# Kernel tuning notes

Hardware: AMD Instinct MI355X
Metric: run time of the kernel (lower is better)

The kernel has to match this reference:

```python
import jax, jax.numpy as jnp
import numpy as np

B, S, D, H, E, K = 2, 2048, 512, 2048, 16, 2
LN_EPS = 1e-5


def setup_inputs() -> dict:
    key = jax.random.key(0)
    ks = jax.random.split(key, 9)
    s_in = 1.0 / np.sqrt(D)
    s_hid = 1.0 / np.sqrt(H)
    return {
        "x": jax.random.normal(ks[0], (B, S, D), dtype=jnp.float32),
        "Wg": jax.random.normal(ks[1], (D, E), dtype=jnp.float32) * s_in,
        "bg": jax.random.normal(ks[2], (E,), dtype=jnp.float32) * 0.01,
        "W1": jax.random.normal(ks[3], (E, D, H), dtype=jnp.float32) * s_in,
        "b1": jax.random.normal(ks[4], (E, H), dtype=jnp.float32) * 0.01,
        "W2": jax.random.normal(ks[5], (E, H, D), dtype=jnp.float32) * s_hid,
        "b2": jax.random.normal(ks[6], (E, D), dtype=jnp.float32) * 0.01,
        "gamma": jnp.ones((D,), dtype=jnp.float32),
        "beta": jnp.zeros((D,), dtype=jnp.float32),
    }


def reference(x, Wg, bg, W1, b1, W2, b2, gamma, beta):
    # --- top-k gating (GatingFuncTopK) ---
    logits = jnp.einsum("bsd,de->bse", x, Wg) + bg            # [B,S,E]
    probs = jax.nn.softmax(logits, axis=-1)
    topk_vals, topk_idx = jax.lax.top_k(probs, K)             # [B,S,K]
    # scatter top-k probs back into a sparse [B,S,E] routing matrix
    sparse = (jax.nn.one_hot(topk_idx, E, dtype=probs.dtype)
              * topk_vals[..., None]).sum(axis=-2)            # [B,S,E]

    # --- dense all-expert FFN (stack over experts, as in the torch code) ---
    h = jax.nn.relu(jnp.einsum("bsd,edh->ebsh", x, W1)
                    + b1[:, None, None, :])                   # [E,B,S,H]
    ex = jnp.einsum("ebsh,ehd->ebsd", h, W2) + b2[:, None, None, :]  # [E,B,S,D]

    # --- weighted combine + residual + layernorm ---
    out = jnp.einsum("bse,ebsd->bsd", sparse, ex) + x
    mu = out.mean(axis=-1, keepdims=True)
    var = ((out - mu) ** 2).mean(axis=-1, keepdims=True)
    out = (out - mu) * jax.lax.rsqrt(var + LN_EPS) * gamma + beta
    return out
```

## Files before the change

### kernel.cpp

```cpp
#include <hip/hip_runtime.h>
#include <math.h>

#define NTOK 4096
#define DDIM 512
#define HDIM 2048
#define NEXP 16


#define WS_COUNTS    0u
#define WS_OFFSETS   1024u
#define WS_NTILES    1280u
#define WS_TM        1536u
#define WS_EPOS      4096u
#define WS_TOK       36864u
#define WS_WL        299008u
#define WS_XA        1048576u
#define WS_W1T       11534336u
#define WS_W2T       45088768u
#define WS_HB        78643200u
#define WS_YB        WS_W1T

typedef __attribute__((ext_vector_type(8))) short short8;
typedef __attribute__((ext_vector_type(4))) float floatx4;
typedef unsigned short ushort_t;

__device__ __forceinline__ ushort_t f2bf(float f) {
    unsigned u = __float_as_uint(f);
    u += 0x7fffu + ((u >> 16) & 1u);
    return (ushort_t)(u >> 16);
}
__device__ __forceinline__ float bf2f(ushort_t u) {
    return __uint_as_float((unsigned)u << 16);
}

__device__ __forceinline__ void gld16(const void* g, void* l) {
    __builtin_amdgcn_global_load_lds(
        (const __attribute__((address_space(1))) unsigned*)g,
        (__attribute__((address_space(3))) unsigned*)l, 16, 0, 0);
}

__device__ __forceinline__ void wtrans_tile(
    const float* __restrict__ src, ushort_t* __restrict__ dst,
    int C, int NT, int CK, int e, int ks, int nw, unsigned* lb, int tid)
{
    const int q = tid >> 4;
    const int c0 = (tid & 15) << 2;
    const float* sp = src + (size_t)e * (DDIM * HDIM)
                    + (size_t)(ks * 32 + 2 * q) * C + nw * 256;
    float4 va[4], vb[4];
    #pragma unroll
    for (int p = 0; p < 4; ++p) {
        va[p] = *(const float4*)(sp + c0 + p * 64);
        vb[p] = *(const float4*)(sp + C + c0 + p * 64);
    }
    #pragma unroll
    for (int p = 0; p < 4; ++p) {
        const int n = c0 + p * 64;
        lb[(n + 0) * 17 + q] = (unsigned)f2bf(va[p].x) | ((unsigned)f2bf(vb[p].x) << 16);
        lb[(n + 1) * 17 + q] = (unsigned)f2bf(va[p].y) | ((unsigned)f2bf(vb[p].y) << 16);
        lb[(n + 2) * 17 + q] = (unsigned)f2bf(va[p].z) | ((unsigned)f2bf(vb[p].z) << 16);
        lb[(n + 3) * 17 + q] = (unsigned)f2bf(va[p].w) | ((unsigned)f2bf(vb[p].w) << 16);
    }
    __syncthreads();
    const int nt = tid >> 4, nl = tid & 15;
    const int ntg = nw * 16 + nt;
    ushort_t* rbase = dst + ((size_t)e * NT + ntg) * ((size_t)CK * 128) + nl * 8;
    const unsigned* rp = lb + (nt * 16 + nl) * 17;
    #pragma unroll
    for (int kc = 0; kc < 4; ++kc) {
        const unsigned o0 = rp[kc * 4 + 0], o1 = rp[kc * 4 + 1];
        const unsigned o2 = rp[kc * 4 + 2], o3 = rp[kc * 4 + 3];
        *(uint4*)(rbase + (size_t)(ks * 4 + kc) * 128) = make_uint4(o0, o1, o2, o3);
    }
}

__global__ __launch_bounds__(256) void fusedA_kernel(
    const float* __restrict__ x, const float* __restrict__ Wg,
    const float* __restrict__ bg, int* __restrict__ counts,
    int* __restrict__ tok_list, float* __restrict__ w_list,
    int* __restrict__ epos, const float* __restrict__ W1,
    ushort_t* __restrict__ W1t)
{
    __shared__ __align__(16) float smem[4416];
    __shared__ int lcnt[16], lbase[16];
    const int tid = threadIdx.x;
    int bid = blockIdx.x;

    if (bid >= 512) {
        bid -= 512;
        const int e = bid >> 7, r = bid & 127;
        const int nw = r & 7, ks = r >> 3;
        wtrans_tile(W1, W1t, HDIM, 128, 64, e, ks, nw, (unsigned*)smem, tid);
        return;
    }

    float (*xs)[520] = (float(*)[520])smem;
    float (*lsm)[16][2] = (float(*)[16][2])(smem + 4160);
    const int t0 = bid * 8;
    const float* xg = x + (size_t)t0 * DDIM;
    #pragma unroll
    for (int p = 0; p < 4; ++p) {
        const int idx = p * 1024 + tid * 4;
        *(float4*)&xs[idx >> 9][idx & 511] = *(const float4*)(xg + idx);
    }
    if (tid < 16) lcnt[tid] = 0;
    __syncthreads();
    const int tl = tid >> 5, e = (tid >> 1) & 15, h = tid & 1;
    float a0 = 0.f, a1 = 0.f, a2 = 0.f, a3 = 0.f;
    #pragma unroll 8
    for (int it = 0; it < 64; ++it) {
        const int d = h * 256 + it * 4;
        const float4 xv = *(const float4*)&xs[tl][d];
        a0 = fmaf(xv.x, Wg[(d + 0) * 16 + e], a0);
        a1 = fmaf(xv.y, Wg[(d + 1) * 16 + e], a1);
        a2 = fmaf(xv.z, Wg[(d + 2) * 16 + e], a2);
        a3 = fmaf(xv.w, Wg[(d + 3) * 16 + e], a3);
    }
    lsm[tl][e][h] = (a0 + a1) + (a2 + a3);
    __syncthreads();

    int i0 = 0, i1 = -1, r0 = 0, r1 = 0;
    float w0 = 0.f, w1 = 0.f;
    const bool tokth = ((tid & 31) == 0);
    if (tokth) {
        float l[16];
        #pragma unroll
        for (int j = 0; j < NEXP; ++j) l[j] = lsm[tl][j][0] + lsm[tl][j][1] + bg[j];
        float m = -1e30f;
        #pragma unroll
        for (int j = 0; j < NEXP; ++j) m = fmaxf(m, l[j]);
        float s = 0.f;
        #pragma unroll
        for (int j = 0; j < NEXP; ++j) s += __expf(l[j] - m);
        float v0 = -1e30f;
        #pragma unroll
        for (int j = 0; j < NEXP; ++j)
            if (l[j] > v0) { v0 = l[j]; i0 = j; }
        float v1 = -1e30f;
        #pragma unroll
        for (int j = 0; j < NEXP; ++j)
            if (j != i0 && l[j] > v1) { v1 = l[j]; i1 = j; }
        w0 = __expf(v0 - m) / s;
        w1 = __expf(v1 - m) / s;
        r0 = atomicAdd(&lcnt[i0], 1);
        r1 = atomicAdd(&lcnt[i1], 1);
    }
    __syncthreads();
    if (tid < 16 && lcnt[tid] > 0)
        lbase[tid] = atomicAdd(&counts[tid * 16], lcnt[tid]);
    __syncthreads();
    if (tokth) {
        const int t = t0 + tl;
        const int p0 = lbase[i0] + r0;
        tok_list[i0 * NTOK + p0] = t;
        w_list[i0 * NTOK + p0] = w0;
        epos[t * 2 + 0] = (i0 << 16) | p0;
        const int p1 = lbase[i1] + r1;
        tok_list[i1 * NTOK + p1] = t;
        w_list[i1 * NTOK + p1] = w1;
        epos[t * 2 + 1] = (i1 << 16) | p1;
    }
}

__global__ void scan_kernel(const int* __restrict__ counts, int* __restrict__ offsets,
                            int* __restrict__ tm, int* __restrict__ ntiles)
{
    const int lane = threadIdx.x;
    int c = (lane < NEXP) ? counts[lane * 16] : 0;
    int t = (c + 127) >> 7;
    int ic = c, it = t;
    #pragma unroll
    for (int off = 1; off < 16; off <<= 1) {
        const int pc = __shfl_up(ic, off, 64);
        const int pt = __shfl_up(it, off, 64);
        if (lane >= off) { ic += pc; it += pt; }
    }
    if (lane < NEXP) {
        offsets[lane] = ic - c;
        if (lane == NEXP - 1) { offsets[NEXP] = ic; ntiles[0] = it; }
        const int tb = it - t;
        for (int i = 0; i < t; ++i) tm[tb + i] = (lane << 16) | i;
    }
}

__global__ __launch_bounds__(256) void gather_xa(
    const float* __restrict__ x, const int* __restrict__ tok_list,
    const int* __restrict__ counts, const int* __restrict__ tm,
    const int* __restrict__ ntiles, ushort_t* __restrict__ xa)
{
    const int b = blockIdx.x;
    if (b >= ntiles[0]) return;
    const int info = tm[b];
    const int e = info >> 16, m0 = (info & 0xffff) << 7;
    const int Me = counts[e * 16];
    const int row = threadIdx.x >> 1;
    const int half = threadIdx.x & 1;
    const int kbase = blockIdx.y * 128 + half * 64;
    const int tok = tok_list[e * NTOK + min(m0 + row, Me - 1)];
    const float* src = x + (size_t)tok * DDIM + kbase;
    ushort_t* dstb = xa + (size_t)b * 65536 + (size_t)(row >> 4) * 8192 + (row & 15) * 8;
    #pragma unroll
    for (int q = 0; q < 16; ++q) {
        const int k = kbase + q * 4;
        const float4 v = *(const float4*)(src + q * 4);
        ushort4 o = make_ushort4(f2bf(v.x), f2bf(v.y), f2bf(v.z), f2bf(v.w));
        *(ushort4*)(dstb + (size_t)(k >> 3) * 128 + (k & 7)) = o;
    }
}

__global__ __launch_bounds__(256) void fusedC_kernel(
    const ushort_t* __restrict__ xa, const ushort_t* __restrict__ W1t,
    const float* __restrict__ b1, const int* __restrict__ tm,
    const int* __restrict__ ntiles, ushort_t* __restrict__ hb,
    const float* __restrict__ W2, ushort_t* __restrict__ W2t)
{
    __shared__ __align__(16) ushort_t lds[16384];
    const int tid = threadIdx.x;
    const int bid = blockIdx.x;

    if (bid >= 1280) {
        const int wb = bid - 1280;
        const int e = wb >> 7, r = wb & 127;
        const int nw = r & 1, ks = r >> 1;
        wtrans_tile(W2, W2t, DDIM, 32, 256, e, ks, nw, (unsigned*)lds, tid);
        return;
    }

    const int t = bid >> 4;
    if (t >= ntiles[0]) return;
    const int e = tm[t] >> 16;
    const int n0 = (bid & 15) << 7;
    const int lane = tid & 63, w = tid >> 6;
    const int fm = lane & 15, fq = lane >> 4;
    const int wr = (w >> 1) << 6, wc = (w & 1) << 6;

    const ushort_t* gA = xa + (size_t)t * 65536 + lane * 8;
    const ushort_t* gB = W1t + ((size_t)e * 128 + (n0 >> 4)) * 8192 + lane * 8;
    const int s0 = w, s1 = w + 4;

    #define G1_STAGE(d, kc) do {                                            \
        ushort_t* lb_ = &lds[(d) * 8192];                                   \
        gld16(gA + (size_t)s0 * 8192 + (kc) * 512, lb_ + s0 * 512);         \
        gld16(gA + (size_t)s1 * 8192 + (kc) * 512, lb_ + s1 * 512);         \
        gld16(gB + (size_t)s0 * 8192 + (kc) * 512, lb_ + 4096 + s0 * 512);  \
        gld16(gB + (size_t)s1 * 8192 + (kc) * 512, lb_ + 4096 + s1 * 512);  \
    } while (0)

    G1_STAGE(0, 0);
    __syncthreads();

    floatx4 acc[4][4] = {};
    for (int kc = 0; kc < 16; ++kc) {
        const int d = kc & 1;
        if (kc < 15) G1_STAGE(d ^ 1, kc + 1);
        const ushort_t* la = &lds[d * 8192 + (wr >> 4) * 512 + lane * 8];
        const ushort_t* lbB = &lds[d * 8192 + 4096 + (wc >> 4) * 512 + lane * 8];
        short8 af[4], bf[4];
        #pragma unroll
        for (int i = 0; i < 4; ++i) af[i] = *(const short8*)(la + i * 512);
        #pragma unroll
        for (int j = 0; j < 4; ++j) bf[j] = *(const short8*)(lbB + j * 512);
        #pragma unroll
        for (int i = 0; i < 4; ++i)
            #pragma unroll
            for (int j = 0; j < 4; ++j)
                acc[i][j] = __builtin_amdgcn_mfma_f32_16x16x32_bf16(
                    af[i], bf[j], acc[i][j], 0, 0, 0);
        __syncthreads();
    }
    #undef G1_STAGE

    ushort_t* ls = lds;
    #pragma unroll
    for (int j = 0; j < 4; ++j) {
        const float bias = b1[(size_t)e * HDIM + n0 + wc + j * 16 + fm];
        #pragma unroll
        for (int i = 0; i < 4; ++i)
            #pragma unroll
            for (int r = 0; r < 4; ++r) {
                const int row = wr + i * 16 + fq * 4 + r;
                ls[row * 128 + wc + j * 16 + fm] =
                    f2bf(fmaxf(acc[i][j][r] + bias, 0.f));
            }
    }
    __syncthreads();
    ushort_t* hbase = hb + (size_t)t * 262144 + (size_t)(n0 >> 3) * 128;
    #pragma unroll
    for (int p = 0; p < 8; ++p) {
        const int unit = tid + p * 256;
        const int row = unit >> 4, c16 = unit & 15;
        *(short8*)(hbase + (size_t)(row >> 4) * 32768 + (size_t)c16 * 128
                   + (row & 15) * 8) = *(const short8*)&ls[row * 128 + c16 * 8];
    }
}

__global__ __launch_bounds__(256) void gemm2_mfma(
    const ushort_t* __restrict__ hb, const ushort_t* __restrict__ W2t,
    const float* __restrict__ b2, const float* __restrict__ w_list,
    const int* __restrict__ counts, const int* __restrict__ offsets,
    const int* __restrict__ tm, const int* __restrict__ ntiles,
    ushort_t* __restrict__ yb)
{
    const int t = blockIdx.y;
    if (t >= ntiles[0]) return;
    const int info = tm[t];
    const int e = info >> 16, m0 = (info & 0xffff) << 7;
    const int Me = counts[e * 16], aoff = offsets[e];
    const int n0 = blockIdx.x << 7;
    const int kz = blockIdx.z;
    const int tid = threadIdx.x, lane = tid & 63, w = tid >> 6;
    const int fm = lane & 15, fq = lane >> 4;
    const int wr = (w >> 1) << 6, wc = (w & 1) << 6;

    __shared__ __align__(16) ushort_t lds[16384];

    const ushort_t* gA = hb + (size_t)t * 262144 + (size_t)kz * 8192 + lane * 8;
    const ushort_t* gB = W2t + ((size_t)e * 32 + (n0 >> 4)) * 32768
                       + (size_t)kz * 8192 + lane * 8;
    const int s0 = w, s1 = w + 4;

    #define G2_STAGE(d, kc) do {                                            \
        ushort_t* lb_ = &lds[(d) * 8192];                                   \
        gld16(gA + (size_t)s0 * 32768 + (kc) * 512, lb_ + s0 * 512);        \
        gld16(gA + (size_t)s1 * 32768 + (kc) * 512, lb_ + s1 * 512);        \
        gld16(gB + (size_t)s0 * 32768 + (kc) * 512, lb_ + 4096 + s0 * 512); \
        gld16(gB + (size_t)s1 * 32768 + (kc) * 512, lb_ + 4096 + s1 * 512); \
    } while (0)

    G2_STAGE(0, 0);
    __syncthreads();

    floatx4 acc[4][4] = {};
    for (int kc = 0; kc < 16; ++kc) {
        const int d = kc & 1;
        if (kc < 15) G2_STAGE(d ^ 1, kc + 1);
        const ushort_t* la = &lds[d * 8192 + (wr >> 4) * 512 + lane * 8];
        const ushort_t* lbB = &lds[d * 8192 + 4096 + (wc >> 4) * 512 + lane * 8];
        short8 af[4], bf[4];
        #pragma unroll
        for (int i = 0; i < 4; ++i) af[i] = *(const short8*)(la + i * 512);
        #pragma unroll
        for (int j = 0; j < 4; ++j) bf[j] = *(const short8*)(lbB + j * 512);
        #pragma unroll
        for (int i = 0; i < 4; ++i)
            #pragma unroll
            for (int j = 0; j < 4; ++j)
                acc[i][j] = __builtin_amdgcn_mfma_f32_16x16x32_bf16(
                    af[i], bf[j], acc[i][j], 0, 0, 0);
        __syncthreads();
    }
    #undef G2_STAGE

    ushort_t* ls = lds;
    #pragma unroll
    for (int j = 0; j < 4; ++j) {
        const float bias = (kz == 0) ? b2[(size_t)e * DDIM + n0 + wc + j * 16 + fm] : 0.f;
        #pragma unroll
        for (int i = 0; i < 4; ++i)
            #pragma unroll
            for (int r = 0; r < 4; ++r) {
                const int row = wr + i * 16 + fq * 4 + r;
                const float gw = w_list[e * NTOK + min(m0 + row, Me - 1)];
                ls[row * 128 + wc + j * 16 + fm] = f2bf(gw * (acc[i][j][r] + bias));
            }
    }
    __syncthreads();
    ushort_t* ybase = yb + (size_t)kz * (8192 * 512) + n0;
    #pragma unroll
    for (int p = 0; p < 8; ++p) {
        const int unit = tid + p * 256;
        const int row = unit >> 4, c16 = unit & 15;
        if (m0 + row < Me)
            *(short8*)(ybase + (size_t)(aoff + m0 + row) * 512 + c16 * 8)
                = *(const short8*)&ls[row * 128 + c16 * 8];
    }
}

__global__ __launch_bounds__(256) void ln_kernel(
    const float* __restrict__ x, const ushort_t* __restrict__ yb,
    const int* __restrict__ epos, const int* __restrict__ offsets,
    const float* __restrict__ gamma, const float* __restrict__ beta,
    float* __restrict__ out)
{
    const int t = blockIdx.x * 4 + (threadIdx.x >> 6);
    const int lane = threadIdx.x & 63;
    const int d0 = lane * 8;

    const int p0 = epos[2 * t + 0];
    const int p1 = epos[2 * t + 1];
    const size_t r0 = (size_t)(offsets[p0 >> 16] + (p0 & 0xFFFF));
    const size_t r1 = (size_t)(offsets[p1 >> 16] + (p1 & 0xFFFF));

    short8 ys[8];
    #pragma unroll
    for (int kz = 0; kz < 4; ++kz) {
        ys[kz * 2 + 0] = *(const short8*)(yb + (size_t)kz * (8192 * 512) + r0 * 512 + d0);
        ys[kz * 2 + 1] = *(const short8*)(yb + (size_t)kz * (8192 * 512) + r1 * 512 + d0);
    }
    float xv[8];
    *(float4*)&xv[0] = *(const float4*)(x + (size_t)t * DDIM + d0);
    *(float4*)&xv[4] = *(const float4*)(x + (size_t)t * DDIM + d0 + 4);

    float v[8];
    float s = 0.f;
    #pragma unroll
    for (int i = 0; i < 8; ++i) {
        float a = xv[i];
        #pragma unroll
        for (int q = 0; q < 8; ++q) a += bf2f((ushort_t)ys[q][i]);
        v[i] = a;
        s += a;
    }
    #pragma unroll
    for (int o = 32; o > 0; o >>= 1) s += __shfl_xor(s, o, 64);
    const float mu = s * (1.f / DDIM);
    float q = 0.f;
    #pragma unroll
    for (int i = 0; i < 8; ++i) { const float d_ = v[i] - mu; q = fmaf(d_, d_, q); }
    #pragma unroll
    for (int o = 32; o > 0; o >>= 1) q += __shfl_xor(q, o, 64);
    const float rstd = rsqrtf(q * (1.f / DDIM) + 1e-5f);

    float g[8], bt[8], o8[8];
    *(float4*)&g[0] = *(const float4*)(gamma + d0);
    *(float4*)&g[4] = *(const float4*)(gamma + d0 + 4);
    *(float4*)&bt[0] = *(const float4*)(beta + d0);
    *(float4*)&bt[4] = *(const float4*)(beta + d0 + 4);
    #pragma unroll
    for (int i = 0; i < 8; ++i) o8[i] = (v[i] - mu) * rstd * g[i] + bt[i];
    *(float4*)(out + (size_t)t * DDIM + d0) = *(float4*)&o8[0];
    *(float4*)(out + (size_t)t * DDIM + d0 + 4) = *(float4*)&o8[4];
}

extern "C" void kernel_launch(void* const* d_in, const int* in_sizes, int n_in,
                              void* d_out, int out_size, void* d_ws, size_t ws_size,
                              hipStream_t stream) {
    const float* x     = (const float*)d_in[0];
    const float* Wg    = (const float*)d_in[1];
    const float* bg    = (const float*)d_in[2];
    const float* W1    = (const float*)d_in[3];
    const float* b1    = (const float*)d_in[4];
    const float* W2    = (const float*)d_in[5];
    const float* b2    = (const float*)d_in[6];
    const float* gamma = (const float*)d_in[7];
    const float* beta  = (const float*)d_in[8];
    float* out = (float*)d_out;

    char* ws = (char*)d_ws;
    int*      counts   = (int*)(ws + WS_COUNTS);
    int*      offsets  = (int*)(ws + WS_OFFSETS);
    int*      ntiles   = (int*)(ws + WS_NTILES);
    int*      tm       = (int*)(ws + WS_TM);
    int*      epos     = (int*)(ws + WS_EPOS);
    int*      tok_list = (int*)(ws + WS_TOK);
    float*    w_list   = (float*)(ws + WS_WL);
    ushort_t* xa       = (ushort_t*)(ws + WS_XA);
    ushort_t* W1t      = (ushort_t*)(ws + WS_W1T);
    ushort_t* W2t      = (ushort_t*)(ws + WS_W2T);
    ushort_t* hb       = (ushort_t*)(ws + WS_HB);
    ushort_t* yb       = (ushort_t*)(ws + WS_YB);

    hipMemsetAsync(counts, 0, 1024, stream);
    fusedA_kernel<<<2560, 256, 0, stream>>>(x, Wg, bg, counts, tok_list, w_list,
                                            epos, W1, W1t);
    scan_kernel<<<1, 64, 0, stream>>>(counts, offsets, tm, ntiles);
    gather_xa<<<dim3(80, 4), 256, 0, stream>>>(x, tok_list, counts, tm, ntiles, xa);
    fusedC_kernel<<<3328, 256, 0, stream>>>(xa, W1t, b1, tm, ntiles, hb, W2, W2t);
    gemm2_mfma<<<dim3(DDIM / 128, 80, 4), 256, 0, stream>>>(
        hb, W2t, b2, w_list, counts, offsets, tm, ntiles, yb);
    ln_kernel<<<NTOK / 4, 256, 0, stream>>>(x, yb, epos, offsets, gamma, beta, out);
}
```

Baseline: 276.5 us.

## Triple-buffer GEMM K-loop with vmcnt waits and swizzle block indices

Both expert GEMM kernels move from a double-buffered LDS pipeline with full syncthreads to a three-stage ring buffer. Each stage waits with an explicit s_waitcnt vmcnt(4) plus barrier, so two async global-to-LDS loads stay in flight while MFMA work runs. Block IDs are remapped with an 8-way XCD-style swizzle, and gemm2 now uses a flat 1D grid, to improve cache locality across chiplets. This raises LDS use per block to 48KB, which may lower occupancy, and relies on hand-counted vmcnt values being correct.

Result: faster. 263.2 us (-4.8%).

```diff
diff --git a/kernel.cpp b/kernel.cpp
--- a/kernel.cpp
+++ b/kernel.cpp
@@ -39,6 +39,9 @@
         (__attribute__((address_space(3))) unsigned*)l, 16, 0, 0);
 }
 
+#define WAIT4_BAR() asm volatile("s_waitcnt vmcnt(4)\n\ts_barrier" ::: "memory")
+#define WAIT0_BAR() asm volatile("s_waitcnt vmcnt(0)\n\ts_barrier" ::: "memory")
+
 __device__ __forceinline__ void wtrans_tile(
     const float* __restrict__ src, ushort_t* __restrict__ dst,
     int C, int NT, int CK, int e, int ks, int nw, unsigned* lb, int tid)
@@ -214,7 +217,7 @@
     const int* __restrict__ ntiles, ushort_t* __restrict__ hb,
     const float* __restrict__ W2, ushort_t* __restrict__ W2t)
 {
-    __shared__ __align__(16) ushort_t lds[16384];
+    __shared__ __align__(16) ushort_t lds[24576];
     const int tid = threadIdx.x;
     const int bid = blockIdx.x;
 
@@ -226,10 +229,11 @@
         return;
     }
 
-    const int t = bid >> 4;
+    const int swz = (bid & 7) * 160 + (bid >> 3);
+    const int t = swz >> 4;
     if (t >= ntiles[0]) return;
     const int e = tm[t] >> 16;
-    const int n0 = (bid & 15) << 7;
+    const int n0 = (swz & 15) << 7;
     const int lane = tid & 63, w = tid >> 6;
     const int fm = lane & 15, fq = lane >> 4;
     const int wr = (w >> 1) << 6, wc = (w & 1) << 6;
@@ -246,29 +250,42 @@
         gld16(gB + (size_t)s1 * 8192 + (kc) * 512, lb_ + 4096 + s1 * 512);  \
     } while (0)
 
+    #define G1_COMPUTE(cur) do {                                            \
+        const ushort_t* la = &lds[(cur) * 8192 + ((w >> 1) * 4) * 512 + lane * 8]; \
+        const ushort_t* lbB = &lds[(cur) * 8192 + 4096 + ((w & 1) * 4) * 512 + lane * 8]; \
+        short8 af[4], bf[4];                                                \
+        _Pragma("unroll")                                                   \
+        for (int i = 0; i < 4; ++i) af[i] = *(const short8*)(la + i * 512); \
+        _Pragma("unroll")                                                   \
+        for (int j = 0; j < 4; ++j) bf[j] = *(const short8*)(lbB + j * 512);\
+        _Pragma("unroll")                                                   \
+        for (int i = 0; i < 4; ++i)                                         \
+            _Pragma("unroll")                                               \
+            for (int j = 0; j < 4; ++j)                                     \
+                acc[i][j] = __builtin_amdgcn_mfma_f32_16x16x32_bf16(        \
+                    af[i], bf[j], acc[i][j], 0, 0, 0);                      \
+    } while (0)
+
     G1_STAGE(0, 0);
-    __syncthreads();
-
+    G1_STAGE(1, 1);
     floatx4 acc[4][4] = {};
-    for (int kc = 0; kc < 16; ++kc) {
-        const int d = kc & 1;
-        if (kc < 15) G1_STAGE(d ^ 1, kc + 1);
-        const ushort_t* la = &lds[d * 8192 + (wr >> 4) * 512 + lane * 8];
-        const ushort_t* lbB = &lds[d * 8192 + 4096 + (wc >> 4) * 512 + lane * 8];
-        short8 af[4], bf[4];
-        #pragma unroll
-        for (int i = 0; i < 4; ++i) af[i] = *(const short8*)(la + i * 512);
-        #pragma unroll
-        for (int j = 0; j < 4; ++j) bf[j] = *(const short8*)(lbB + j * 512);
-        #pragma unroll
-        for (int i = 0; i < 4; ++i)
-            #pragma unroll
-            for (int j = 0; j < 4; ++j)
-                acc[i][j] = __builtin_amdgcn_mfma_f32_16x16x32_bf16(
-                    af[i], bf[j], acc[i][j], 0, 0, 0);
-        __syncthreads();
-    }
+    int cur = 0;
+    #pragma unroll 1
+    for (int kc = 0; kc < 14; ++kc) {
+        WAIT4_BAR();
+        const int nb = (kc + 2) % 3;
+        G1_STAGE(nb, kc + 2);
+        G1_COMPUTE(cur);
+        cur = (cur == 2) ? 0 : cur + 1;
+    }
+    WAIT4_BAR();
+    G1_COMPUTE(cur);
+    cur = (cur == 2) ? 0 : cur + 1;
+    WAIT0_BAR();
+    G1_COMPUTE(cur);
+    __syncthreads();
     #undef G1_STAGE
+    #undef G1_COMPUTE
 
     ushort_t* ls = lds;
     #pragma unroll
@@ -301,18 +318,22 @@
     const int* __restrict__ tm, const int* __restrict__ ntiles,
     ushort_t* __restrict__ yb)
 {
-    const int t = blockIdx.y;
+    const int bid = blockIdx.x;
+    const int swz = (bid & 7) * 160 + (bid >> 3);
+    const int n0i = swz & 3;
+    const int q = swz >> 2;
+    const int kz = q / 80;
+    const int t = q - kz * 80;
     if (t >= ntiles[0]) return;
     const int info = tm[t];
     const int e = info >> 16, m0 = (info & 0xffff) << 7;
     const int Me = counts[e * 16], aoff = offsets[e];
-    const int n0 = blockIdx.x << 7;
-    const int kz = blockIdx.z;
+    const int n0 = n0i << 7;
     const int tid = threadIdx.x, lane = tid & 63, w = tid >> 6;
     const int fm = lane & 15, fq = lane >> 4;
     const int wr = (w >> 1) << 6, wc = (w & 1) << 6;
 
-    __shared__ __align__(16) ushort_t lds[16384];
+    __shared__ __align__(16) ushort_t lds[24576];
 
     const ushort_t* gA = hb + (size_t)t * 262144 + (size_t)kz * 8192 + lane * 8;
     const ushort_t* gB = W2t + ((size_t)e * 32 + (n0 >> 4)) * 32768
@@ -327,29 +348,42 @@
         gld16(gB + (size_t)s1 * 32768 + (kc) * 512, lb_ + 4096 + s1 * 512); \
     } while (0)
 
+    #define G2_COMPUTE(cur) do {                                            \
+        const ushort_t* la = &lds[(cur) * 8192 + ((w >> 1) * 4) * 512 + lane * 8]; \
+        const ushort_t* lbB = &lds[(cur) * 8192 + 4096 + ((w & 1) * 4) * 512 + lane * 8]; \
+        short8 af[4], bf[4];                                                \
+        _Pragma("unroll")                                                   \
+        for (int i = 0; i < 4; ++i) af[i] = *(const short8*)(la + i * 512); \
+        _Pragma("unroll")                                                   \
+        for (int j = 0; j < 4; ++j) bf[j] = *(const short8*)(lbB + j * 512);\
+        _Pragma("unroll")                                                   \
+        for (int i = 0; i < 4; ++i)                                         \
+            _Pragma("unroll")                                               \
+            for (int j = 0; j < 4; ++j)                                     \
+                acc[i][j] = __builtin_amdgcn_mfma_f32_16x16x32_bf16(        \
+                    af[i], bf[j], acc[i][j], 0, 0, 0);                      \
+    } while (0)
+
     G2_STAGE(0, 0);
-    __syncthreads();
-
+    G2_STAGE(1, 1);
     floatx4 acc[4][4] = {};
-    for (int kc = 0; kc < 16; ++kc) {
-        const int d = kc & 1;
-        if (kc < 15) G2_STAGE(d ^ 1, kc + 1);
-        const ushort_t* la = &lds[d * 8192 + (wr >> 4) * 512 + lane * 8];
-        const ushort_t* lbB = &lds[d * 8192 + 4096 + (wc >> 4) * 512 + lane * 8];
-        short8 af[4], bf[4];
-        #pragma unroll
-        for (int i = 0; i < 4; ++i) af[i] = *(const short8*)(la + i * 512);
-        #pragma unroll
-        for (int j = 0; j < 4; ++j) bf[j] = *(const short8*)(lbB + j * 512);
-        #pragma unroll
-        for (int i = 0; i < 4; ++i)
-            #pragma unroll
-            for (int j = 0; j < 4; ++j)
-                acc[i][j] = __builtin_amdgcn_mfma_f32_16x16x32_bf16(
-                    af[i], bf[j], acc[i][j], 0, 0, 0);
-        __syncthreads();
-    }
+    int cur = 0;
+    #pragma unroll 1
+    for (int kc = 0; kc < 14; ++kc) {
+        WAIT4_BAR();
+        const int nb = (kc + 2) % 3;
+        G2_STAGE(nb, kc + 2);
+        G2_COMPUTE(cur);
+        cur = (cur == 2) ? 0 : cur + 1;
+    }
+    WAIT4_BAR();
+    G2_COMPUTE(cur);
+    cur = (cur == 2) ? 0 : cur + 1;
+    WAIT0_BAR();
+    G2_COMPUTE(cur);
+    __syncthreads();
     #undef G2_STAGE
+    #undef G2_COMPUTE
 
     ushort_t* ls = lds;
     #pragma unroll
@@ -466,7 +500,7 @@
     scan_kernel<<<1, 64, 0, stream>>>(counts, offsets, tm, ntiles);
     gather_xa<<<dim3(80, 4), 256, 0, stream>>>(x, tok_list, counts, tm, ntiles, xa);
     fusedC_kernel<<<3328, 256, 0, stream>>>(xa, W1t, b1, tm, ntiles, hb, W2, W2t);
-    gemm2_mfma<<<dim3(DDIM / 128, 80, 4), 256, 0, stream>>>(
+    gemm2_mfma<<<1280, 256, 0, stream>>>(
         hb, W2t, b2, w_list, counts, offsets, tm, ntiles, yb);
     ln_kernel<<<NTOK / 4, 256, 0, stream>>>(x, yb, epos, offsets, gamma, beta, out);
 }
```
